# Kernel optimization log

Measured on AMD Instinct MI355X. Metric: run time of the kernel, lower is better.

Reference implementation:

```python
import jax, jax.numpy as jnp
import numpy as np

NUM_HEADS = 8
RADIUS = 127          # local_attention_radius -> block_length = 128
RMAX = 64             # rel_pos_max_distance -> R = 2*RMAX+1 = 129


def setup_inputs() -> dict:
    key = jax.random.key(0)
    ks = jax.random.split(key, 9)
    B, S, D = 2, 4096, 512
    hd = D // NUM_HEADS
    R = 2 * RMAX + 1
    w = lambda k, shape: 0.02 * jax.random.normal(k, shape, jnp.float32)
    return {
        "Q": jax.random.normal(ks[0], (B, S, D), jnp.float32),
        "K": jax.random.normal(ks[1], (B, S, D), jnp.float32),
        "V": jax.random.normal(ks[2], (B, S, D), jnp.float32),
        "segment_ids": jnp.zeros((B, S), jnp.int32),
        "Wq": w(ks[3], (D, D)),
        "Wk": w(ks[4], (D, D)),
        "Wv": w(ks[5], (D, D)),
        "Wo": w(ks[6], (D, D)),
        "rel_emb": w(ks[7], (NUM_HEADS, R, hd)),
    }


def reference(Q, K, V, segment_ids, Wq, Wk, Wv, Wo, rel_emb):
    B, S, D = Q.shape
    h = NUM_HEADS
    hd = D // h
    bl = RADIUS + 1                      # block length
    nb = -(-S // bl)                     # num query blocks
    pad = nb * bl - S                    # 0 for S divisible by bl
    norm = float(hd) ** 0.5

    def proj(X, W):  # B x S x D -> B x h x S x hd
        return (X @ W).reshape(B, S, h, hd).transpose(0, 2, 1, 3)

    q = proj(Q, Wq)
    k = proj(K, Wk)
    v = proj(V, Wv)

    # query blocks: B x h x nb x bl x hd
    qb = jnp.pad(q, ((0, 0), (0, 0), (0, pad), (0, 0))).reshape(B, h, nb, bl, hd)
    # sliding key/value blocks: pad bl on each side, gather 3*bl window per block
    kp = jnp.pad(k, ((0, 0), (0, 0), (bl, bl + pad), (0, 0)))
    vp = jnp.pad(v, ((0, 0), (0, 0), (bl, bl + pad), (0, 0)))
    slid = jnp.arange(3 * bl)[None, :] + bl * jnp.arange(nb)[:, None]  # nb x 3bl
    kb = kp[:, :, slid, :]  # B x h x nb x 3bl x hd
    vb = vp[:, :, slid, :]

    energy = jnp.einsum("bhnqd,bhnkd->bhnqk", qb, kb)  # B x h x nb x bl x 3bl

    # relative position bias: Q @ rel_embeds^T then gather by rel pos ids
    qrel = jnp.einsum("bhnqd,hrd->bhnqr", qb, rel_emb)  # B x h x nb x bl x R
    i = jnp.arange(bl)
    j = jnp.arange(3 * bl)
    dpos = j[None, :] - bl - i[:, None]                 # bl x 3bl, key - query offset
    ids = jnp.clip(dpos, -RMAX, RMAX) + RMAX            # bl x 3bl in [0, 2*RMAX]
    rel_shift = qrel[:, :, :, i[:, None], ids]          # B x h x nb x bl x 3bl

    energy = (energy + rel_shift) / norm

    # mask: out-of-sequence keys and keys beyond local radius
    kg = bl * jnp.arange(nb)[:, None, None] + (j - bl)[None, None, :]
    invalid = (kg < 0) | (kg >= S) | (jnp.abs(dpos)[None] > RADIUS)    # nb x bl x 3bl
    energy = jnp.where(invalid[None, None], -jnp.inf, energy)

    attn = jax.nn.softmax(energy, axis=-1)
    outb = jnp.einsum("bhnqk,bhnkd->bhnqd", attn, vb)   # B x h x nb x bl x hd
    out = outb.reshape(B, h, nb * bl, hd)[:, :, :S, :]  # B x h x S x hd
    # torch code interleaves features as (head_dim, head): permute(0,2,3,1).flatten(2,3)
    out = out.transpose(0, 2, 3, 1).reshape(B, S, hd * h)
    return out @ Wo
```

## Files before the change

### kernel.cpp

```cpp
#include <hip/hip_runtime.h>
#include <hip/hip_bf16.h>

typedef unsigned short u16;
typedef __bf16 bf16_t;
typedef bf16_t bf16x8 __attribute__((ext_vector_type(8)));
typedef float f32x4 __attribute__((ext_vector_type(4)));
typedef u16 u16x4 __attribute__((ext_vector_type(4)));
typedef u16 u16x8 __attribute__((ext_vector_type(8)));

#define S_LEN 4096
#define NH 8
#define HD 64
#define DM 512
#define NB 32

__device__ __forceinline__ u16 f2bf(float f) {
  unsigned int u = __builtin_bit_cast(unsigned int, f);
  u = (u + 0x7fff + ((u >> 16) & 1)) >> 16;
  return (u16)u;
}
__device__ __forceinline__ float bf2f(u16 h) {
  unsigned int u = ((unsigned int)h) << 16;
  return __builtin_bit_cast(float, u);
}

#define GLDS16(gaddr, laddr)                                                  \
  __builtin_amdgcn_global_load_lds(                                           \
      (const __attribute__((address_space(1))) unsigned int*)(gaddr),         \
      (__attribute__((address_space(3))) unsigned int*)(laddr), 16, 0, 0)

__global__ __launch_bounds__(256) void conv_big(
    const float* __restrict__ Q, const float* __restrict__ K,
    const float* __restrict__ V, u16* __restrict__ Qb, u16* __restrict__ Kb,
    u16* __restrict__ Vb) {
  const int z = blockIdx.y;
  const float* src = z == 0 ? Q : (z == 1 ? K : V);
  u16* dst = z == 0 ? Qb : (z == 1 ? Kb : Vb);
  const size_t idx = ((size_t)blockIdx.x * 256 + threadIdx.x) * 4;
  const float4 v = *(const float4*)(src + idx);
  u16x4 o;
  o[0] = f2bf(v.x); o[1] = f2bf(v.y); o[2] = f2bf(v.z); o[3] = f2bf(v.w);
  *(u16x4*)(dst + idx) = o;
}

__global__ __launch_bounds__(256) void conv_w(
    const float* __restrict__ Wq, const float* __restrict__ Wk,
    const float* __restrict__ Wv, const float* __restrict__ Wo,
    u16* __restrict__ WqT, u16* __restrict__ WkT, u16* __restrict__ WvT,
    u16* __restrict__ WoT) {
  const int z = blockIdx.y;
  const float* src = z == 0 ? Wq : (z == 1 ? Wk : (z == 2 ? Wv : Wo));
  u16* dst = z == 0 ? WqT : (z == 1 ? WkT : (z == 2 ? WvT : WoT));
  const float scl = (z == 0) ? 0.125f : 1.f;
  const int idx4 = blockIdx.x * 256 + threadIdx.x;
  const int nrow = idx4 >> 7;
  const int kbase = (idx4 & 127) * 4;
  u16x4 o;
#pragma unroll
  for (int j = 0; j < 4; ++j) {
    const int k = kbase + j;
    const int srow = (z == 3) ? ((k & 63) * 8 + (k >> 6)) : k;
    o[j] = f2bf(src[srow * DM + nrow] * scl);
  }
  *(u16x4*)(dst + nrow * DM + kbase) = o;
}

__global__ __launch_bounds__(128) void conv_rel(const float* __restrict__ rel,
                                                u16* __restrict__ relb) {
  const int e = (blockIdx.x * 128 + threadIdx.x) * 4;
  const int h = e / (129 * 64);
  const int rem = e - h * (129 * 64);
  const float4 v = *(const float4*)(rel + e);
  u16x4 o;
  o[0] = f2bf(v.x); o[1] = f2bf(v.y); o[2] = f2bf(v.z); o[3] = f2bf(v.w);
  *(u16x4*)(relb + (size_t)h * (144 * 64) + rem) = o;
}

template <int MODE>
__global__ __launch_bounds__(256, 2) void gemm_bf16(
    const u16* __restrict__ A0, const u16* __restrict__ A1,
    const u16* __restrict__ A2, const u16* __restrict__ B0,
    const u16* __restrict__ B1, const u16* __restrict__ B2,
    u16* __restrict__ C0, u16* __restrict__ C1, u16* __restrict__ C2,
    float* __restrict__ Cf) {
  __shared__ u16 As[2][128 * 32];
  __shared__ u16 Bs[2][128 * 32];

  const int z = blockIdx.z;
  const u16* A = (MODE == 1) ? (z == 0 ? A0 : (z == 1 ? A1 : A2)) : A0;
  const u16* Bt = (MODE == 1) ? (z == 0 ? B0 : (z == 1 ? B1 : B2)) : B0;
  u16* Cb = (MODE == 1) ? (z == 0 ? C0 : (z == 1 ? C1 : C2)) : (u16*)0;

  const int tid = threadIdx.x;
  const int lane = tid & 63;
  const int w = tid >> 6;
  const int bm = blockIdx.x * 128;
  const int bn = blockIdx.y * 128;

  const int srow = lane >> 2;
  const int scol = (lane & 3) * 8;

  f32x4 acc[4][4];
#pragma unroll
  for (int m = 0; m < 4; ++m)
#pragma unroll
    for (int nf = 0; nf < 4; ++nf) acc[m][nf] = f32x4{0.f, 0.f, 0.f, 0.f};

  const int wr = w >> 1, wc = w & 1;
  const int lrow = lane & 15;
  const int lk = (lane >> 4) * 8;

  auto stage = [&](int buf, int k0) {
#pragma unroll
    for (int t = 0; t < 2; ++t) {
      const int c = t * 4 + w;
      const int ar = c * 16 + srow;
      long gidx;
      if (MODE == 2) {
        const int r = bm + ar;
        const int b = r >> 12, s = r & 4095;
        const int k = k0 + scol;
        gidx = ((long)((b * 8 + (k >> 6)) * 4096 + s)) * 64 + (k & 63);
      } else {
        gidx = (long)(bm + ar) * DM + k0 + scol;
      }
      GLDS16(A + gidx, &As[buf][c * 512]);
      const long bidx = (long)(bn + ar) * DM + k0 + scol;
      GLDS16(Bt + bidx, &Bs[buf][c * 512]);
    }
  };

  stage(0, 0);
  __syncthreads();

  for (int t = 0; t < 16; ++t) {
    const int cur = t & 1;
    if (t < 15) stage(cur ^ 1, (t + 1) * 32);

    bf16x8 af[4], bfr[4];
#pragma unroll
    for (int m = 0; m < 4; ++m)
      af[m] = *(const bf16x8*)&As[cur][(wr * 64 + m * 16 + lrow) * 32 + lk];
#pragma unroll
    for (int nf = 0; nf < 4; ++nf)
      bfr[nf] = *(const bf16x8*)&Bs[cur][(wc * 64 + nf * 16 + lrow) * 32 + lk];
#pragma unroll
    for (int m = 0; m < 4; ++m)
#pragma unroll
      for (int nf = 0; nf < 4; ++nf)
        acc[m][nf] = __builtin_amdgcn_mfma_f32_16x16x32_bf16(
            bfr[nf], af[m], acc[m][nf], 0, 0, 0);
    __syncthreads();
  }

  const int lr4 = (lane >> 4) * 4;
  const int lc = lane & 15;
#pragma unroll
  for (int m = 0; m < 4; ++m) {
    const int r = bm + wr * 64 + m * 16 + lc;
    const int bi = r >> 12, s = r & 4095;
#pragma unroll
    for (int nf = 0; nf < 4; ++nf) {
      const int cg = bn + wc * 64 + nf * 16 + lr4;
      if (MODE == 1) {
        u16x4 o;
#pragma unroll
        for (int j = 0; j < 4; ++j) o[j] = f2bf(acc[m][nf][j]);
        *(u16x4*)&Cb[((long)((bi * 8 + (cg >> 6)) * 4096 + s)) * 64 +
                     (cg & 63)] = o;
      } else {
        float4 o;
        o.x = acc[m][nf][0]; o.y = acc[m][nf][1];
        o.z = acc[m][nf][2]; o.w = acc[m][nf][3];
        *(float4*)&Cf[(long)r * DM + cg] = o;
      }
    }
  }
}

__global__ __launch_bounds__(256, 2) void attn_mfma(
    const u16* __restrict__ qg, const u16* __restrict__ kgl,
    const u16* __restrict__ vgl, const u16* __restrict__ relb,
    u16* __restrict__ pre) {
  const int n = blockIdx.x, hh = blockIdx.y, b = blockIdx.z;
  const int tid = threadIdx.x;
  const int lane = tid & 63, w = tid >> 6;
  const int g = lane >> 4, lc = lane & 15;

  __shared__ u16 Ks[64 * 72];
  __shared__ u16 Vt[64 * 72];
  __shared__ u16 Pl[4][32 * 72];
  __shared__ u16 qrelL[128 * 132];

  const size_t bh = (size_t)(b * NH + hh);

  const u16* qbase = qg + (bh * S_LEN + (size_t)n * 128 + w * 32) * HD;
  bf16x8 qf[2][2];
#pragma unroll
  for (int qt = 0; qt < 2; ++qt)
#pragma unroll
    for (int dc = 0; dc < 2; ++dc)
      qf[qt][dc] =
          *(const bf16x8*)(qbase + (lc + 16 * qt) * HD + g * 8 + 32 * dc);

  const u16* rh = relb + (size_t)hh * (144 * 64);
#pragma unroll
  for (int rt = 0; rt < 9; ++rt) {
    f32x4 acc[2] = {{0.f, 0.f, 0.f, 0.f}, {0.f, 0.f, 0.f, 0.f}};
#pragma unroll
    for (int dc = 0; dc < 2; ++dc) {
      const bf16x8 rf =
          *(const bf16x8*)(rh + (lc + 16 * rt) * 64 + g * 8 + 32 * dc);
#pragma unroll
      for (int qt = 0; qt < 2; ++qt)
        acc[qt] = __builtin_amdgcn_mfma_f32_16x16x32_bf16(qf[qt][dc], rf,
                                                          acc[qt], 0, 0, 0);
    }
#pragma unroll
    for (int qt = 0; qt < 2; ++qt)
#pragma unroll
      for (int jj = 0; jj < 4; ++jj)
        qrelL[(w * 32 + qt * 16 + g * 4 + jj) * 132 + lc + 16 * rt] =
            f2bf(acc[qt][jj]);
  }

  float m_r[2][4], l_r[2][4];
  f32x4 Oa[2][4];
#pragma unroll
  for (int qt = 0; qt < 2; ++qt)
#pragma unroll
    for (int jj = 0; jj < 4; ++jj) {
      m_r[qt][jj] = -1e30f;
      l_r[qt][jj] = 0.f;
    }
#pragma unroll
  for (int qt = 0; qt < 2; ++qt)
#pragma unroll
    for (int dt = 0; dt < 4; ++dt) Oa[qt][dt] = f32x4{0.f, 0.f, 0.f, 0.f};

  const u16* kbase = kgl + bh * S_LEN * HD;
  const u16* vbase = vgl + bh * S_LEN * HD;
  const int sk = tid & 63;
  const int sd = (tid >> 6) * 16;

  const int t0 = (n == 0) ? 2 : 0;
  const int t1 = (n == NB - 1) ? 4 : 6;

  for (int t = t0; t < t1; ++t) {
    {
      const int kglob = n * 128 - 128 + t * 64 + sk;
      const int kc = min(max(kglob, 0), S_LEN - 1);
      const u16* krow = kbase + (size_t)kc * HD + sd;
      const u16* vrow = vbase + (size_t)kc * HD + sd;
      const u16x8 ka = *(const u16x8*)krow;
      const u16x8 kb2 = *(const u16x8*)(krow + 8);
      const u16x8 va = *(const u16x8*)vrow;
      const u16x8 vb2 = *(const u16x8*)(vrow + 8);
      *(u16x8*)&Ks[sk * 72 + sd] = ka;
      *(u16x8*)&Ks[sk * 72 + sd + 8] = kb2;
#pragma unroll
      for (int e = 0; e < 8; ++e) {
        Vt[(sd + e) * 72 + sk] = va[e];
        Vt[(sd + 8 + e) * 72 + sk] = vb2[e];
      }
    }
    __syncthreads();

    f32x4 E[2][4];
#pragma unroll
    for (int qt = 0; qt < 2; ++qt)
#pragma unroll
      for (int kt = 0; kt < 4; ++kt) E[qt][kt] = f32x4{0.f, 0.f, 0.f, 0.f};
#pragma unroll
    for (int kt = 0; kt < 4; ++kt)
#pragma unroll
      for (int dc = 0; dc < 2; ++dc) {
        const bf16x8 kf =
            *(const bf16x8*)&Ks[(lc + 16 * kt) * 72 + g * 8 + 32 * dc];
#pragma unroll
        for (int qt = 0; qt < 2; ++qt)
          E[qt][kt] = __builtin_amdgcn_mfma_f32_16x16x32_bf16(
              qf[qt][dc], kf, E[qt][kt], 0, 0, 0);
      }

#pragma unroll
    for (int qt = 0; qt < 2; ++qt)
#pragma unroll
      for (int jj = 0; jj < 4; ++jj) {
        const int q = w * 32 + qt * 16 + g * 4 + jj;
#pragma unroll
        for (int kt = 0; kt < 4; ++kt) {
          const int j = t * 64 + kt * 16 + lc;
          const int dpos = j - 128 - q;
          const int idc = min(max(dpos, -64), 64) + 64;
          const float bias = bf2f(qrelL[q * 132 + idc]);
          const float e = E[qt][kt][jj] + bias;
          const bool bad = ((unsigned)(dpos + 127) > 254u);
          E[qt][kt][jj] = bad ? -1e30f : e;
        }
      }

    float mxv[2][4];
    bool loc = true;
#pragma unroll
    for (int qt = 0; qt < 2; ++qt)
#pragma unroll
      for (int jj = 0; jj < 4; ++jj) {
        float mx = fmaxf(fmaxf(E[qt][0][jj], E[qt][1][jj]),
                         fmaxf(E[qt][2][jj], E[qt][3][jj]));
        mx = fmaxf(mx, __shfl_xor(mx, 1));
        mx = fmaxf(mx, __shfl_xor(mx, 2));
        mx = fmaxf(mx, __shfl_xor(mx, 4));
        mx = fmaxf(mx, __shfl_xor(mx, 8));
        mxv[qt][jj] = mx;
        loc = loc && (mx <= m_r[qt][jj] + 8.f);
      }
    if (!__all(loc)) {
#pragma unroll
      for (int qt = 0; qt < 2; ++qt)
#pragma unroll
        for (int jj = 0; jj < 4; ++jj) {
          const float nm = fmaxf(m_r[qt][jj], mxv[qt][jj]);
          const float sc = __expf(m_r[qt][jj] - nm);
          m_r[qt][jj] = nm;
          l_r[qt][jj] *= sc;
#pragma unroll
          for (int dt = 0; dt < 4; ++dt) Oa[qt][dt][jj] *= sc;
        }
    }
#pragma unroll
    for (int qt = 0; qt < 2; ++qt)
#pragma unroll
      for (int jj = 0; jj < 4; ++jj) {
        float ps = 0.f;
#pragma unroll
        for (int kt = 0; kt < 4; ++kt) {
          const float p = __expf(E[qt][kt][jj] - m_r[qt][jj]);
          ps += p;
          Pl[w][(qt * 16 + g * 4 + jj) * 72 + lc + 16 * kt] = f2bf(p);
        }
        ps += __shfl_xor(ps, 1);
        ps += __shfl_xor(ps, 2);
        ps += __shfl_xor(ps, 4);
        ps += __shfl_xor(ps, 8);
        l_r[qt][jj] += ps;
      }
    __syncthreads();

#pragma unroll
    for (int c = 0; c < 2; ++c) {
      bf16x8 pf[2];
#pragma unroll
      for (int qt = 0; qt < 2; ++qt)
        pf[qt] = *(const bf16x8*)&Pl[w][(lc + 16 * qt) * 72 + g * 8 + 32 * c];
#pragma unroll
      for (int dt = 0; dt < 4; ++dt) {
        const bf16x8 vf =
            *(const bf16x8*)&Vt[(lc + 16 * dt) * 72 + g * 8 + 32 * c];
#pragma unroll
        for (int qt = 0; qt < 2; ++qt)
          Oa[qt][dt] = __builtin_amdgcn_mfma_f32_16x16x32_bf16(
              pf[qt], vf, Oa[qt][dt], 0, 0, 0);
      }
    }
    __syncthreads();
  }

  u16* prow = pre + (bh * S_LEN + (size_t)n * 128 + w * 32) * HD;
#pragma unroll
  for (int qt = 0; qt < 2; ++qt)
#pragma unroll
    for (int jj = 0; jj < 4; ++jj) {
      const float inv = 1.f / l_r[qt][jj];
      const int row = qt * 16 + g * 4 + jj;
#pragma unroll
      for (int dt = 0; dt < 4; ++dt)
        prow[row * HD + lc + 16 * dt] = f2bf(Oa[qt][dt][jj] * inv);
    }
}

extern "C" void kernel_launch(void* const* d_in, const int* in_sizes, int n_in,
                              void* d_out, int out_size, void* d_ws,
                              size_t ws_size, hipStream_t stream) {
  const float* Q = (const float*)d_in[0];
  const float* K = (const float*)d_in[1];
  const float* V = (const float*)d_in[2];
  const float* Wq = (const float*)d_in[4];
  const float* Wk = (const float*)d_in[5];
  const float* Wv = (const float*)d_in[6];
  const float* Wo = (const float*)d_in[7];
  const float* rel = (const float*)d_in[8];
  float* out = (float*)d_out;

  const size_t NE = 4194304;
  u16* ws16 = (u16*)d_ws;
  u16* Qb = ws16;
  u16* Kb = Qb + NE;
  u16* Vb = Kb + NE;
  u16* qb = Vb + NE;
  u16* kb = qb + NE;
  u16* vb = kb + NE;
  u16* WqT = vb + NE;
  u16* WkT = WqT + 262144;
  u16* WvT = WkT + 262144;
  u16* WoT = WvT + 262144;
  u16* relb = WoT + 262144;
  u16* pre = Qb;

  conv_big<<<dim3(4096, 3), 256, 0, stream>>>(Q, K, V, Qb, Kb, Vb);
  conv_w<<<dim3(256, 4), 256, 0, stream>>>(Wq, Wk, Wv, Wo, WqT, WkT, WvT, WoT);
  conv_rel<<<dim3(129), 128, 0, stream>>>(rel, relb);
  gemm_bf16<1><<<dim3(64, 4, 3), 256, 0, stream>>>(Qb, Kb, Vb, WqT, WkT, WvT,
                                                   qb, kb, vb, nullptr);
  attn_mfma<<<dim3(NB, NH, 2), 256, 0, stream>>>(qb, kb, vb, relb, pre);
  gemm_bf16<2><<<dim3(64, 4, 1), 256, 0, stream>>>(
      pre, nullptr, nullptr, WoT, nullptr, nullptr, nullptr, nullptr, nullptr,
      out);
}
```

Before: 185.0 us.

## Fuse fp32-to-bf16 input conversion into projection GEMM and shrink GEMM tile

Drops the separate conv_big kernel. The QKV projection GEMM now loads fp32 activations directly, converts them to bf16 in registers and writes them to LDS, which removes a full write and re-read of the bf16 copies. The GEMM M tile is halved to 64, doubling the grid, and occupancy is raised to 4 blocks per CU. The attention kernel gains an explicit out-of-sequence key mask and drops the lazy-rescale check in the online softmax, so the rescale now runs every step. This costs some extra exp work in exchange for simpler control flow.

```diff
diff --git a/kernel.cpp b/kernel.cpp
--- a/kernel.cpp
+++ b/kernel.cpp
@@ -28,20 +28,6 @@
   __builtin_amdgcn_global_load_lds(                                           \
       (const __attribute__((address_space(1))) unsigned int*)(gaddr),         \
       (__attribute__((address_space(3))) unsigned int*)(laddr), 16, 0, 0)
-
-__global__ __launch_bounds__(256) void conv_big(
-    const float* __restrict__ Q, const float* __restrict__ K,
-    const float* __restrict__ V, u16* __restrict__ Qb, u16* __restrict__ Kb,
-    u16* __restrict__ Vb) {
-  const int z = blockIdx.y;
-  const float* src = z == 0 ? Q : (z == 1 ? K : V);
-  u16* dst = z == 0 ? Qb : (z == 1 ? Kb : Vb);
-  const size_t idx = ((size_t)blockIdx.x * 256 + threadIdx.x) * 4;
-  const float4 v = *(const float4*)(src + idx);
-  u16x4 o;
-  o[0] = f2bf(v.x); o[1] = f2bf(v.y); o[2] = f2bf(v.z); o[3] = f2bf(v.w);
-  *(u16x4*)(dst + idx) = o;
-}
 
 __global__ __launch_bounds__(256) void conv_w(
     const float* __restrict__ Wq, const float* __restrict__ Wk,
@@ -77,87 +63,116 @@
 }
 
 template <int MODE>
-__global__ __launch_bounds__(256, 2) void gemm_bf16(
-    const u16* __restrict__ A0, const u16* __restrict__ A1,
-    const u16* __restrict__ A2, const u16* __restrict__ B0,
-    const u16* __restrict__ B1, const u16* __restrict__ B2,
-    u16* __restrict__ C0, u16* __restrict__ C1, u16* __restrict__ C2,
-    float* __restrict__ Cf) {
-  __shared__ u16 As[2][128 * 32];
+__global__ __launch_bounds__(256, 4) void gemm_bf16(
+    const float* __restrict__ Af0, const float* __restrict__ Af1,
+    const float* __restrict__ Af2, const u16* __restrict__ Ab,
+    const u16* __restrict__ B0, const u16* __restrict__ B1,
+    const u16* __restrict__ B2, u16* __restrict__ C0, u16* __restrict__ C1,
+    u16* __restrict__ C2, float* __restrict__ Cf) {
+  __shared__ u16 As[2][64 * 32];
   __shared__ u16 Bs[2][128 * 32];
 
   const int z = blockIdx.z;
-  const u16* A = (MODE == 1) ? (z == 0 ? A0 : (z == 1 ? A1 : A2)) : A0;
+  const float* Af = (MODE == 1) ? (z == 0 ? Af0 : (z == 1 ? Af1 : Af2)) : 0;
   const u16* Bt = (MODE == 1) ? (z == 0 ? B0 : (z == 1 ? B1 : B2)) : B0;
   u16* Cb = (MODE == 1) ? (z == 0 ? C0 : (z == 1 ? C1 : C2)) : (u16*)0;
 
   const int tid = threadIdx.x;
   const int lane = tid & 63;
   const int w = tid >> 6;
-  const int bm = blockIdx.x * 128;
+  const int bm = blockIdx.x * 64;
   const int bn = blockIdx.y * 128;
 
-  const int srow = lane >> 2;
-  const int scol = (lane & 3) * 8;
-
-  f32x4 acc[4][4];
-#pragma unroll
-  for (int m = 0; m < 4; ++m)
-#pragma unroll
-    for (int nf = 0; nf < 4; ++nf) acc[m][nf] = f32x4{0.f, 0.f, 0.f, 0.f};
+  f32x4 acc[2][4];
+#pragma unroll
+  for (int mf = 0; mf < 2; ++mf)
+#pragma unroll
+    for (int nf = 0; nf < 4; ++nf) acc[mf][nf] = f32x4{0.f, 0.f, 0.f, 0.f};
 
   const int wr = w >> 1, wc = w & 1;
   const int lrow = lane & 15;
   const int lk = (lane >> 4) * 8;
 
-  auto stage = [&](int buf, int k0) {
-#pragma unroll
-    for (int t = 0; t < 2; ++t) {
-      const int c = t * 4 + w;
-      const int ar = c * 16 + srow;
-      long gidx;
-      if (MODE == 2) {
-        const int r = bm + ar;
-        const int b = r >> 12, s = r & 4095;
-        const int k = k0 + scol;
-        gidx = ((long)((b * 8 + (k >> 6)) * 4096 + s)) * 64 + (k & 63);
-      } else {
-        gidx = (long)(bm + ar) * DM + k0 + scol;
-      }
-      GLDS16(A + gidx, &As[buf][c * 512]);
-      const long bidx = (long)(bn + ar) * DM + k0 + scol;
-      GLDS16(Bt + bidx, &Bs[buf][c * 512]);
+  const int arow = tid >> 2;
+  const int ac8 = (tid & 3) * 8;
+  const long aoff = (long)(bm + arow) * DM + ac8;
+
+  auto stageB = [&](int buf, int k0) {
+#pragma unroll
+    for (int c = 0; c < 2; ++c) {
+      const int brow = bn + c * 64 + w * 16 + (lane >> 2);
+      GLDS16(Bt + (long)brow * DM + k0 + (lane & 3) * 8,
+             &Bs[buf][c * 2048 + w * 512]);
     }
   };
-
-  stage(0, 0);
-  __syncthreads();
-
-  for (int t = 0; t < 16; ++t) {
-    const int cur = t & 1;
-    if (t < 15) stage(cur ^ 1, (t + 1) * 32);
-
-    bf16x8 af[4], bfr[4];
-#pragma unroll
-    for (int m = 0; m < 4; ++m)
-      af[m] = *(const bf16x8*)&As[cur][(wr * 64 + m * 16 + lrow) * 32 + lk];
+  auto stageA2 = [&](int buf, int k0) {
+    const int r = bm + w * 16 + (lane >> 2);
+    const int b = r >> 12, s = r & 4095;
+    const int k = k0 + (lane & 3) * 8;
+    GLDS16(Ab + ((long)((b * 8 + (k >> 6)) * 4096 + s)) * 64 + (k & 63),
+           &As[buf][w * 512]);
+  };
+  auto writeA = [&](int buf, float4 x0, float4 x1) {
+    u16x8 o;
+    o[0] = f2bf(x0.x); o[1] = f2bf(x0.y); o[2] = f2bf(x0.z); o[3] = f2bf(x0.w);
+    o[4] = f2bf(x1.x); o[5] = f2bf(x1.y); o[6] = f2bf(x1.z); o[7] = f2bf(x1.w);
+    *(u16x8*)&As[buf][arow * 32 + ac8] = o;
+  };
+
+  auto compute = [&](int cur) {
+    bf16x8 af[2], bfr[4];
+#pragma unroll
+    for (int mf = 0; mf < 2; ++mf)
+      af[mf] = *(const bf16x8*)&As[cur][(wr * 32 + mf * 16 + lrow) * 32 + lk];
 #pragma unroll
     for (int nf = 0; nf < 4; ++nf)
       bfr[nf] = *(const bf16x8*)&Bs[cur][(wc * 64 + nf * 16 + lrow) * 32 + lk];
 #pragma unroll
-    for (int m = 0; m < 4; ++m)
+    for (int mf = 0; mf < 2; ++mf)
 #pragma unroll
       for (int nf = 0; nf < 4; ++nf)
-        acc[m][nf] = __builtin_amdgcn_mfma_f32_16x16x32_bf16(
-            bfr[nf], af[m], acc[m][nf], 0, 0, 0);
+        acc[mf][nf] = __builtin_amdgcn_mfma_f32_16x16x32_bf16(
+            bfr[nf], af[mf], acc[mf][nf], 0, 0, 0);
+  };
+
+  if constexpr (MODE == 1) {
+    float4 c0 = *(const float4*)&Af[aoff];
+    float4 c1 = *(const float4*)&Af[aoff + 4];
+    stageB(0, 0);
+    writeA(0, c0, c1);
     __syncthreads();
+    for (int t = 0; t < 16; ++t) {
+      const int cur = t & 1;
+      float4 n0, n1;
+      if (t < 15) {
+        n0 = *(const float4*)&Af[aoff + (t + 1) * 32];
+        n1 = *(const float4*)&Af[aoff + (t + 1) * 32 + 4];
+        stageB(cur ^ 1, (t + 1) * 32);
+      }
+      compute(cur);
+      if (t < 15) writeA(cur ^ 1, n0, n1);
+      __syncthreads();
+    }
+  } else {
+    stageA2(0, 0);
+    stageB(0, 0);
+    __syncthreads();
+    for (int t = 0; t < 16; ++t) {
+      const int cur = t & 1;
+      if (t < 15) {
+        stageA2(cur ^ 1, (t + 1) * 32);
+        stageB(cur ^ 1, (t + 1) * 32);
+      }
+      compute(cur);
+      __syncthreads();
+    }
   }
 
   const int lr4 = (lane >> 4) * 4;
   const int lc = lane & 15;
 #pragma unroll
-  for (int m = 0; m < 4; ++m) {
-    const int r = bm + wr * 64 + m * 16 + lc;
+  for (int mf = 0; mf < 2; ++mf) {
+    const int r = bm + wr * 32 + mf * 16 + lc;
     const int bi = r >> 12, s = r & 4095;
 #pragma unroll
     for (int nf = 0; nf < 4; ++nf) {
@@ -165,13 +180,13 @@
       if (MODE == 1) {
         u16x4 o;
 #pragma unroll
-        for (int j = 0; j < 4; ++j) o[j] = f2bf(acc[m][nf][j]);
+        for (int j = 0; j < 4; ++j) o[j] = f2bf(acc[mf][nf][j]);
         *(u16x4*)&Cb[((long)((bi * 8 + (cg >> 6)) * 4096 + s)) * 64 +
                      (cg & 63)] = o;
       } else {
         float4 o;
-        o.x = acc[m][nf][0]; o.y = acc[m][nf][1];
-        o.z = acc[m][nf][2]; o.w = acc[m][nf][3];
+        o.x = acc[mf][nf][0]; o.y = acc[mf][nf][1];
+        o.z = acc[mf][nf][2]; o.w = acc[mf][nf][3];
         *(float4*)&Cf[(long)r * DM + cg] = o;
       }
     }
@@ -292,16 +307,16 @@
         for (int kt = 0; kt < 4; ++kt) {
           const int j = t * 64 + kt * 16 + lc;
           const int dpos = j - 128 - q;
+          const int kglob = n * 128 - 128 + j;
           const int idc = min(max(dpos, -64), 64) + 64;
           const float bias = bf2f(qrelL[q * 132 + idc]);
           const float e = E[qt][kt][jj] + bias;
-          const bool bad = ((unsigned)(dpos + 127) > 254u);
+          const bool bad = (dpos > 127) || (dpos < -127) ||
+                           ((unsigned)kglob >= (unsigned)S_LEN);
           E[qt][kt][jj] = bad ? -1e30f : e;
         }
       }
 
-    float mxv[2][4];
-    bool loc = true;
 #pragma unroll
     for (int qt = 0; qt < 2; ++qt)
 #pragma unroll
@@ -312,30 +327,16 @@
         mx = fmaxf(mx, __shfl_xor(mx, 2));
         mx = fmaxf(mx, __shfl_xor(mx, 4));
         mx = fmaxf(mx, __shfl_xor(mx, 8));
-        mxv[qt][jj] = mx;
-        loc = loc && (mx <= m_r[qt][jj] + 8.f);
-      }
-    if (!__all(loc)) {
-#pragma unroll
-      for (int qt = 0; qt < 2; ++qt)
-#pragma unroll
-        for (int jj = 0; jj < 4; ++jj) {
-          const float nm = fmaxf(m_r[qt][jj], mxv[qt][jj]);
-          const float sc = __expf(m_r[qt][jj] - nm);
-          m_r[qt][jj] = nm;
-          l_r[qt][jj] *= sc;
-#pragma unroll
-          for (int dt = 0; dt < 4; ++dt) Oa[qt][dt][jj] *= sc;
-        }
-    }
-#pragma unroll
-    for (int qt = 0; qt < 2; ++qt)
-#pragma unroll
-      for (int jj = 0; jj < 4; ++jj) {
+        const float nm = fmaxf(m_r[qt][jj], mx);
+        const float sc = __expf(m_r[qt][jj] - nm);
+        m_r[qt][jj] = nm;
+        l_r[qt][jj] *= sc;
+#pragma unroll
+        for (int dt = 0; dt < 4; ++dt) Oa[qt][dt][jj] *= sc;
         float ps = 0.f;
 #pragma unroll
         for (int kt = 0; kt < 4; ++kt) {
-          const float p = __expf(E[qt][kt][jj] - m_r[qt][jj]);
+          const float p = __expf(E[qt][kt][jj] - nm);
           ps += p;
           Pl[w][(qt * 16 + g * 4 + jj) * 72 + lc + 16 * kt] = f2bf(p);
         }
@@ -394,26 +395,22 @@
 
   const size_t NE = 4194304;
   u16* ws16 = (u16*)d_ws;
-  u16* Qb = ws16;
-  u16* Kb = Qb + NE;
-  u16* Vb = Kb + NE;
-  u16* qb = Vb + NE;
+  u16* qb = ws16;
   u16* kb = qb + NE;
   u16* vb = kb + NE;
-  u16* WqT = vb + NE;
+  u16* pre = vb + NE;
+  u16* WqT = pre + NE;
   u16* WkT = WqT + 262144;
   u16* WvT = WkT + 262144;
   u16* WoT = WvT + 262144;
   u16* relb = WoT + 262144;
-  u16* pre = Qb;
-
-  conv_big<<<dim3(4096, 3), 256, 0, stream>>>(Q, K, V, Qb, Kb, Vb);
+
   conv_w<<<dim3(256, 4), 256, 0, stream>>>(Wq, Wk, Wv, Wo, WqT, WkT, WvT, WoT);
   conv_rel<<<dim3(129), 128, 0, stream>>>(rel, relb);
-  gemm_bf16<1><<<dim3(64, 4, 3), 256, 0, stream>>>(Qb, Kb, Vb, WqT, WkT, WvT,
-                                                   qb, kb, vb, nullptr);
+  gemm_bf16<1><<<dim3(128, 4, 3), 256, 0, stream>>>(
+      Q, K, V, nullptr, WqT, WkT, WvT, qb, kb, vb, nullptr);
   attn_mfma<<<dim3(NB, NH, 2), 256, 0, stream>>>(qb, kb, vb, relb, pre);
-  gemm_bf16<2><<<dim3(64, 4, 1), 256, 0, stream>>>(
-      pre, nullptr, nullptr, WoT, nullptr, nullptr, nullptr, nullptr, nullptr,
-      out);
-}
+  gemm_bf16<2><<<dim3(128, 4, 1), 256, 0, stream>>>(
+      nullptr, nullptr, nullptr, pre, WoT, nullptr, nullptr, nullptr, nullptr,
+      nullptr, out);
+}
```

Result: slower. 193.4 us (+4.5%).
